# Optimization experiments

Measured on AMD Instinct MI355X. Metric: run time of the kernel, lower is better.

The kernel has to match this reference:

```python
import jax, jax.numpy as jnp
import numpy as np

NUM_REL = 5000
NUM_BIN = 32
NUM_EDGES = 200000
DIM = 512
NUM_HEAD = 8
DIM_HID = DIM // NUM_HEAD


def setup_inputs() -> dict:
    key = jax.random.key(0)
    ks = jax.random.split(key, 10)
    emb_rel = jax.random.normal(ks[0], (NUM_REL, DIM), dtype=jnp.float32)
    emb_bin = jax.random.normal(ks[1], (NUM_BIN, DIM), dtype=jnp.float32)
    head = jax.random.randint(ks[2], (NUM_EDGES, 1), 0, NUM_REL)
    tail = jax.random.randint(ks[3], (NUM_EDGES, 1), 0, NUM_REL)
    bins = jax.random.randint(ks[4], (NUM_EDGES, 1), 0, NUM_BIN)
    relation_triplets = jnp.concatenate([head, tail, bins], axis=1).astype(jnp.int64)
    gain = float(np.sqrt(2.0))  # calculate_gain('relu')
    # xavier normal: std = gain * sqrt(2/(fan_in+fan_out))
    std_attn = gain * np.sqrt(2.0 / (3 * DIM + DIM))
    std_aggr = gain * np.sqrt(2.0 / (DIM + DIM))
    std_vec = gain * np.sqrt(2.0 / (NUM_HEAD + DIM_HID))
    W_attn = std_attn * jax.random.normal(ks[5], (DIM, 3 * DIM), dtype=jnp.float32)
    b_attn = jnp.zeros((DIM,), dtype=jnp.float32)
    attn_vec = std_vec * jax.random.normal(ks[6], (1, NUM_HEAD, DIM_HID), dtype=jnp.float32)
    W_aggr = std_aggr * jax.random.normal(ks[7], (DIM, DIM), dtype=jnp.float32)
    b_aggr = jnp.zeros((DIM,), dtype=jnp.float32)
    return {"emb_rel": emb_rel, "emb_bin": emb_bin, "relation_triplets": relation_triplets,
            "W_attn": W_attn, "b_attn": b_attn, "attn_vec": attn_vec,
            "W_aggr": W_aggr, "b_aggr": b_aggr}


def reference(emb_rel, emb_bin, relation_triplets, W_attn, b_attn, attn_vec, W_aggr, b_aggr):
    num_rel = emb_rel.shape[0]
    head = relation_triplets[:, 0]
    tail = relation_triplets[:, 1]
    bins = relation_triplets[:, 2]
    # gather + concat -> [E, 3*D]
    concat = jnp.concatenate([emb_rel[head], emb_bin[bins], emb_rel[tail]], axis=-1)
    h = jax.nn.leaky_relu(concat @ W_attn.T + b_attn, negative_slope=0.2)
    h = h.reshape(-1, NUM_HEAD, DIM_HID)
    attn_raw = jnp.sum(h * attn_vec, axis=-1)  # [E, H]
    # segmented softmax over edges sharing the same head relation
    seg_max = jax.ops.segment_max(attn_raw, head, num_segments=num_rel)  # [R, H]
    seg_max = jnp.where(jnp.isfinite(seg_max), seg_max, 0.0)  # empty segments
    ev = jnp.exp(attn_raw - seg_max[head])  # [E, H]
    seg_sum = jax.ops.segment_sum(ev, head, num_segments=num_rel)  # [R, H]
    beta = ev / (seg_sum[head] + 1e-16)  # [E, H]
    msg = (emb_rel[tail] @ W_aggr.T + b_aggr).reshape(-1, NUM_HEAD, DIM_HID)  # [E, H, Dh]
    out = jax.ops.segment_sum(beta[..., None] * msg, head, num_segments=num_rel)  # [R, H, Dh]
    return out.reshape(num_rel, -1)
```

## Files before the change

### kernel.cpp

```cpp
#include <hip/hip_runtime.h>
#include <hip/hip_bf16.h>

#define NREL 5000
#define NBIN 32
#define NEDGE 200000
#define DIM 512
#define NHEAD 8
#define CAP 256

typedef __attribute__((ext_vector_type(8))) short short8;
typedef __attribute__((ext_vector_type(4))) short short4v;
typedef __attribute__((ext_vector_type(4))) float f32x4;
typedef unsigned short ushort_t;

#define REL_N (NREL * DIM)
#define BIN_N (NBIN * DIM)
#define WATTN_N (DIM * 3 * DIM)
#define WAGGR_N (DIM * DIM)
#define CTOT (REL_N + BIN_N + WATTN_N + WAGGR_N)
#define CONV_BLOCKS (CTOT / 4 / 256)

__device__ __forceinline__ float b2f(ushort_t u) {
  unsigned int v = ((unsigned int)u) << 16;
  union { unsigned int i; float f; } c; c.i = v; return c.f;
}
__device__ __forceinline__ ushort_t f2b_rne(float f) {
  union { float f; unsigned int u; } c; c.f = f;
  unsigned int u = c.u;
  return (ushort_t)((u + 0x7FFFu + ((u >> 16) & 1u)) >> 16);
}
__device__ __forceinline__ void gload16(const void* g, void* l) {
  __builtin_amdgcn_global_load_lds(
      (const __attribute__((address_space(1))) void*)g,
      (__attribute__((address_space(3))) void*)l, 16, 0, 0);
}

__global__ void conv_k(const float* __restrict__ s_rel, const float* __restrict__ s_bin,
                       const float* __restrict__ s_wattn, const float* __restrict__ s_waggr,
                       ushort_t* __restrict__ dst, int* __restrict__ cur) {
  int b = blockIdx.x;
  if (b < 20) {
    int i = b * 256 + threadIdx.x;
    if (i < NREL) cur[i] = 0;
  }
  const int O1 = REL_N, O2 = O1 + BIN_N, O3 = O2 + WATTN_N;
  int i4 = (b * 256 + threadIdx.x) * 4;
  const float* src; int j;
  if (i4 < O1)      { src = s_rel;   j = i4; }
  else if (i4 < O2) { src = s_bin;   j = i4 - O1; }
  else if (i4 < O3) { src = s_wattn; j = i4 - O2; }
  else              { src = s_waggr; j = i4 - O3; }
  float4 v = *(const float4*)(src + j);
  short4v o;
  o[0] = (short)f2b_rne(v.x); o[1] = (short)f2b_rne(v.y);
  o[2] = (short)f2b_rne(v.z); o[3] = (short)f2b_rne(v.w);
  *(short4v*)(dst + i4) = o;
}

__global__ __launch_bounds__(256) void gemm_scatter_k(
    const ushort_t* __restrict__ c_rel, const ushort_t* __restrict__ c_bin,
    const ushort_t* __restrict__ c_wattn, const float* __restrict__ b_attn,
    const ushort_t* __restrict__ c_waggr, const float* __restrict__ b_aggr,
    ushort_t* __restrict__ P1B, ushort_t* __restrict__ PM, ushort_t* __restrict__ P2,
    const int* __restrict__ trip, int* __restrict__ cur, unsigned int* __restrict__ etb)
{
  __shared__ ushort_t Alds[64 * 64];
  __shared__ ushort_t Blds[128 * 64];
  int bx = blockIdx.x, by = blockIdx.y;
  if (by >= 12) {
    int sid = (by - 12) * 80 + bx;
    for (int i = threadIdx.x; i < 625; i += 256) {
      int e = sid * 625 + i;
      int h  = trip[3 * e];
      int ta = trip[3 * e + 1];
      int bi = trip[3 * e + 2];
      h  = min(max(h, 0), NREL - 1);
      ta = min(max(ta, 0), NREL - 1);
      bi = min(max(bi, 0), NBIN - 1);
      int p = atomicAdd(&cur[h], 1);
      if (p < CAP)
        etb[(h << 8) + p] = ((unsigned int)ta << 11) | ((unsigned int)bi << 24);
    }
    return;
  }
  const ushort_t* A; int Arows;
  const ushort_t* Bbase; int Bld; int joff;
  const float* bias;
  ushort_t* OUT; int OUTld; int ocolOff;
  int rbase;
  if (bx == 79) {
    if (by >= 4) return;
    A = c_bin; Arows = NBIN; rbase = 0;
    Bbase = c_wattn + 512; Bld = 3 * DIM; joff = 0;
    bias = b_attn;
    OUT = P2; OUTld = DIM; ocolOff = 0;
  } else {
    A = c_rel; Arows = NREL; rbase = bx * 64;
    int seg = by >> 2;
    if (seg == 2)      { Bbase = c_waggr;        Bld = DIM;     bias = b_aggr; }
    else if (seg == 1) { Bbase = c_wattn + 1024; Bld = 3 * DIM; bias = nullptr; }
    else               { Bbase = c_wattn;        Bld = 3 * DIM; bias = nullptr; }
    joff = seg * 512;
    OUT = (seg == 0) ? P1B : PM;
    OUTld = (seg == 0) ? DIM : 1024;
    ocolOff = (seg == 0) ? 0 : 512;
  }
  int tid = threadIdx.x;
  int l = tid & 63, wv = tid >> 6;
  int ctb = by * 128;
  int lr = l >> 3;
  int srcslot = (l & 7) ^ lr;
  const ushort_t* aS0; const ushort_t* aS1;
  const ushort_t* bS0; const ushort_t* bS1; const ushort_t* bS2; const ushort_t* bS3;
  {
    int a0 = wv * 16 + 0 * 8 + lr, a1 = wv * 16 + 1 * 8 + lr;
    aS0 = A + (size_t)min(rbase + a0, Arows - 1) * DIM + srcslot * 8;
    aS1 = A + (size_t)min(rbase + a1, Arows - 1) * DIM + srcslot * 8;
    int c0 = wv * 32 + 0 * 8 + lr, c1 = wv * 32 + 1 * 8 + lr,
        c2 = wv * 32 + 2 * 8 + lr, c3 = wv * 32 + 3 * 8 + lr;
    bS0 = Bbase + (size_t)(ctb + c0 - joff) * Bld + srcslot * 8;
    bS1 = Bbase + (size_t)(ctb + c1 - joff) * Bld + srcslot * 8;
    bS2 = Bbase + (size_t)(ctb + c2 - joff) * Bld + srcslot * 8;
    bS3 = Bbase + (size_t)(ctb + c3 - joff) * Bld + srcslot * 8;
  }
  ushort_t* aD0 = Alds + (wv * 16 + 0) * 64;
  ushort_t* aD1 = Alds + (wv * 16 + 8) * 64;
  ushort_t* bD0 = Blds + (wv * 32 + 0) * 64;
  ushort_t* bD1 = Blds + (wv * 32 + 8) * 64;
  ushort_t* bD2 = Blds + (wv * 32 + 16) * 64;
  ushort_t* bD3 = Blds + (wv * 32 + 24) * 64;

  f32x4 acc[4][2] = {};
  for (int kk = 0; kk < DIM; kk += 64) {
    gload16(aS0 + kk, aD0); gload16(aS1 + kk, aD1);
    gload16(bS0 + kk, bD0); gload16(bS1 + kk, bD1);
    gload16(bS2 + kk, bD2); gload16(bS3 + kk, bD3);
    __syncthreads();
#pragma unroll
    for (int ks = 0; ks < 2; ++ks) {
      int sg = ks * 4 + (l >> 4);
      int sw = (sg ^ (l & 7)) * 8;
      short8 aF[4], bF[2];
#pragma unroll
      for (int m2 = 0; m2 < 4; ++m2) {
        int mrow = m2 * 16 + (l & 15);
        aF[m2] = *(const short8*)(Alds + mrow * 64 + sw);
      }
#pragma unroll
      for (int n = 0; n < 2; ++n) {
        int crow = wv * 32 + n * 16 + (l & 15);
        bF[n] = *(const short8*)(Blds + crow * 64 + sw);
      }
#pragma unroll
      for (int m2 = 0; m2 < 4; ++m2)
#pragma unroll
        for (int n = 0; n < 2; ++n)
          acc[m2][n] = __builtin_amdgcn_mfma_f32_16x16x32_bf16(aF[m2], bF[n], acc[m2][n], 0, 0, 0);
    }
    __syncthreads();
  }
  int r0 = rbase + (l >> 4) * 4;
#pragma unroll
  for (int n = 0; n < 2; ++n) {
    int col = ctb + wv * 32 + n * 16 + (l & 15);
    float bv = bias ? bias[col - joff] : 0.0f;
    int ocol = col - ocolOff;
#pragma unroll
    for (int m2 = 0; m2 < 4; ++m2) {
#pragma unroll
      for (int jj = 0; jj < 4; ++jj) {
        int row = r0 + m2 * 16 + jj;
        if (row < Arows) OUT[(size_t)row * OUTld + ocol] = f2b_rne(acc[m2][n][jj] + bv);
      }
    }
  }
}

#define EDGE_LOAD(TB, P2V, P3V, MV)                                     \
  {                                                                     \
    const char* row_ = PMc + ((TB) & 0x00FFFFFFu);                      \
    P2V = *(const short8*)(p2lds + (((TB) >> 24) << 10) + l16);         \
    P3V = *(const short8*)(row_ + l16);                                 \
    MV  = *(const short8*)(row_ + 1024 + l16);                          \
  }

#define EDGE_COMPUTE(P2V, P3V, MV)                                      \
  {                                                                     \
    float part = 0.0f;                                                  \
    _Pragma("unroll")                                                   \
    for (int j = 0; j < 8; ++j) {                                       \
      float z = p1v[j] + b2f((ushort_t)P2V[j]) + b2f((ushort_t)P3V[j]); \
      part += z * (z > 0.f ? avv[j] : avv02[j]);                        \
    }                                                                   \
    part += __shfl_xor(part, 1);                                        \
    part += __shfl_xor(part, 2);                                        \
    part += __shfl_xor(part, 4);                                        \
    if (part > m + 8.0f) {                                              \
      float f = __expf(m - part);                                       \
      s *= f;                                                           \
      _Pragma("unroll")                                                 \
      for (int j = 0; j < 8; ++j) acc[j] *= f;                          \
      m = part;                                                         \
    }                                                                   \
    float ev = __expf(part - m);                                        \
    s += ev;                                                            \
    _Pragma("unroll")                                                   \
    for (int j = 0; j < 8; ++j) acc[j] += ev * b2f((ushort_t)MV[j]);    \
  }

__global__ __launch_bounds__(256, 6) void aggr2_k(
    const int* __restrict__ cur, const unsigned int* __restrict__ etb,
    const ushort_t* __restrict__ P1B, const ushort_t* __restrict__ PM,
    const ushort_t* __restrict__ P2, const float* __restrict__ avec,
    float* __restrict__ outf)
{
  __shared__ __align__(16) char shmem[32 * DIM * 2];

  int t = threadIdx.x;
  int l = t & 63, wv = t >> 6;
  int p = wv >> 1, sub = wv & 1;
  int r = blockIdx.x * 2 + p;
  int nE = min(cur[r], CAP);
  int base = r << 8;
  int half = nE >> 1;
  int start = sub ? half : 0;
  int cnt = sub ? (nE - half) : half;

  int hd1 = l >> 3;
  int ob = l * 8;
  int l16 = l * 16;

  {
    ushort_t* p2dst = (ushort_t*)shmem;
#pragma unroll
    for (int i = 0; i < 8; ++i) {
      int idx = t * 8 + i * 2048;
      *(short8*)(p2dst + idx) = *(const short8*)(P2 + idx);
    }
  }

  float p1v[8], avv[8], avv02[8];
  {
    short8 p1b = *(const short8*)(P1B + (size_t)r * DIM + ob);
#pragma unroll
    for (int j = 0; j < 8; ++j) {
      p1v[j] = b2f((ushort_t)p1b[j]);
      float a = avec[ob + j];
      avv[j] = a;
      avv02[j] = 0.2f * a;
    }
  }
  float acc[8] = {};
  float m = -INFINITY, s = 0.0f;

  const char* PMc = (const char*)PM;
  const char* p2lds = (const char*)shmem;

  __syncthreads();

  for (int ck = 0; ck < cnt; ck += 64) {
    int ne = min(64, cnt - ck);
    unsigned int tbreg = 0;
    if (l < ne) tbreg = etb[base + start + ck + l];
    short8 p2A, p3A, mvA, p2B, p3B, mvB;
    unsigned int tb0 = (unsigned int)__shfl((int)tbreg, 0);
    EDGE_LOAD(tb0, p2A, p3A, mvA);
    int i = 0;
    while (i + 1 < ne) {
      unsigned int tbb = (unsigned int)__shfl((int)tbreg, i + 1);
      EDGE_LOAD(tbb, p2B, p3B, mvB);
      EDGE_COMPUTE(p2A, p3A, mvA);
      if (i + 2 < ne) {
        unsigned int tba = (unsigned int)__shfl((int)tbreg, i + 2);
        EDGE_LOAD(tba, p2A, p3A, mvA);
      }
      EDGE_COMPUTE(p2B, p3B, mvB);
      i += 2;
    }
    if (i < ne) EDGE_COMPUTE(p2A, p3A, mvA);
  }

  __syncthreads();
  float* red = (float*)shmem;
  float* ms  = (float*)(shmem + 8192);
#pragma unroll
  for (int j = 0; j < 8; ++j) red[wv * DIM + ob + j] = acc[j];
  if ((l & 7) == 0) { ms[(wv * NHEAD + hd1) * 2] = m; ms[(wv * NHEAD + hd1) * 2 + 1] = s; }
  __syncthreads();

  int pp = t >> 7;
  int d0 = (t & 127) * 4;
  int h = d0 >> 6;
  int rr = blockIdx.x * 2 + pp;
  float m1 = ms[((2 * pp) * NHEAD + h) * 2],     s1 = ms[((2 * pp) * NHEAD + h) * 2 + 1];
  float m2 = ms[((2 * pp + 1) * NHEAD + h) * 2], s2 = ms[((2 * pp + 1) * NHEAD + h) * 2 + 1];
  float M = fmaxf(m1, m2);
  float c1 = (m1 == M) ? 1.0f : __expf(m1 - M);
  float c2 = (m2 == M) ? 1.0f : __expf(m2 - M);
  float S = s1 * c1 + s2 * c2;
  float inv = 1.0f / (S + 1e-16f);
  float4 val;
  val.x = (red[(2 * pp) * DIM + d0]     * c1 + red[(2 * pp + 1) * DIM + d0]     * c2) * inv;
  val.y = (red[(2 * pp) * DIM + d0 + 1] * c1 + red[(2 * pp + 1) * DIM + d0 + 1] * c2) * inv;
  val.z = (red[(2 * pp) * DIM + d0 + 2] * c1 + red[(2 * pp + 1) * DIM + d0 + 2] * c2) * inv;
  val.w = (red[(2 * pp) * DIM + d0 + 3] * c1 + red[(2 * pp + 1) * DIM + d0 + 3] * c2) * inv;
  *(float4*)(outf + (size_t)rr * DIM + d0) = val;
}

extern "C" void kernel_launch(void* const* d_in, const int* in_sizes, int n_in,
                              void* d_out, int out_size, void* d_ws, size_t ws_size,
                              hipStream_t stream) {
  const float* s_rel   = (const float*)d_in[0];
  const float* s_bin   = (const float*)d_in[1];
  const int*   trip    = (const int*)d_in[2];
  const float* s_wattn = (const float*)d_in[3];
  const float* b_attn  = (const float*)d_in[4];
  const float* avec    = (const float*)d_in[5];
  const float* s_waggr = (const float*)d_in[6];
  const float* b_aggr  = (const float*)d_in[7];

  ushort_t* canon = (ushort_t*)d_ws;
  ushort_t* c_rel   = canon;
  ushort_t* c_bin   = c_rel + REL_N;
  ushort_t* c_wattn = c_bin + BIN_N;
  ushort_t* c_waggr = c_wattn + WATTN_N;
  int* cur = (int*)(c_waggr + WAGGR_N);
  unsigned int* etb = (unsigned int*)(cur + NREL);
  ushort_t* P1B = (ushort_t*)(((uintptr_t)(etb + NREL * CAP) + 15) & ~(uintptr_t)15);
  ushort_t* PM  = P1B + (size_t)NREL * DIM;
  ushort_t* P2  = PM + (size_t)NREL * 1024;

  conv_k<<<CONV_BLOCKS, 256, 0, stream>>>(s_rel, s_bin, s_wattn, s_waggr, canon, cur);

  dim3 gg(80, 16);
  gemm_scatter_k<<<gg, 256, 0, stream>>>(c_rel, c_bin, c_wattn, b_attn, c_waggr, b_aggr,
                                         P1B, PM, P2, trip, cur, etb);

  aggr2_k<<<NREL / 2, 256, 0, stream>>>(cur, etb, P1B, PM, P2, avec, (float*)d_out);
}
```

Measured before the change: 82.38 us.

## Split fused online-softmax aggregation into logit pass and weighted-sum pass

The single online-softmax aggregation kernel is split in two. The first kernel computes attention logits per edge, writes them to a workspace buffer and produces a per-relation max and sum. The second kernel rereads the edge list and the message rows and accumulates already-normalized weights, so the running rescale of the accumulators is no longer needed. In exchange it adds a kernel launch, rereads etb, PM rows and the logits from memory, and halves CAP to 128, which silently drops edges for any relation with more than 128 incoming edges.

Measured after the change: 97.96 us. 18.9% more time.

```diff
diff --git a/kernel.cpp b/kernel.cpp
--- a/kernel.cpp
+++ b/kernel.cpp
@@ -6,7 +6,7 @@
 #define NEDGE 200000
 #define DIM 512
 #define NHEAD 8
-#define CAP 256
+#define CAP 128
 
 typedef __attribute__((ext_vector_type(8))) short short8;
 typedef __attribute__((ext_vector_type(4))) short short4v;
@@ -79,7 +79,7 @@
       bi = min(max(bi, 0), NBIN - 1);
       int p = atomicAdd(&cur[h], 1);
       if (p < CAP)
-        etb[(h << 8) + p] = ((unsigned int)ta << 11) | ((unsigned int)bi << 24);
+        etb[h * CAP + p] = ((unsigned int)ta << 11) | ((unsigned int)bi << 24);
     }
     return;
   }
@@ -176,15 +176,14 @@
   }
 }
 
-#define EDGE_LOAD(TB, P2V, P3V, MV)                                     \
+#define EDGE_LOAD_A(TB, P2V, P3V)                                       \
   {                                                                     \
     const char* row_ = PMc + ((TB) & 0x00FFFFFFu);                      \
     P2V = *(const short8*)(p2lds + (((TB) >> 24) << 10) + l16);         \
     P3V = *(const short8*)(row_ + l16);                                 \
-    MV  = *(const short8*)(row_ + 1024 + l16);                          \
-  }
-
-#define EDGE_COMPUTE(P2V, P3V, MV)                                      \
+  }
+
+#define EDGE_COMPUTE_A(P2V, P3V, SLOT)                                  \
   {                                                                     \
     float part = 0.0f;                                                  \
     _Pragma("unroll")                                                   \
@@ -196,23 +195,18 @@
     part += __shfl_xor(part, 2);                                        \
     part += __shfl_xor(part, 4);                                        \
     if (part > m + 8.0f) {                                              \
-      float f = __expf(m - part);                                       \
-      s *= f;                                                           \
-      _Pragma("unroll")                                                 \
-      for (int j = 0; j < 8; ++j) acc[j] *= f;                          \
+      s *= __expf(m - part);                                            \
       m = part;                                                         \
     }                                                                   \
-    float ev = __expf(part - m);                                        \
-    s += ev;                                                            \
-    _Pragma("unroll")                                                   \
-    for (int j = 0; j < 8; ++j) acc[j] += ev * b2f((ushort_t)MV[j]);    \
-  }
-
-__global__ __launch_bounds__(256, 6) void aggr2_k(
+    s += __expf(part - m);                                              \
+    if ((l & 7) == 0) LG[(SLOT) * 8 + hd1] = part;                      \
+  }
+
+__global__ __launch_bounds__(256, 6) void aggrA_k(
     const int* __restrict__ cur, const unsigned int* __restrict__ etb,
     const ushort_t* __restrict__ P1B, const ushort_t* __restrict__ PM,
     const ushort_t* __restrict__ P2, const float* __restrict__ avec,
-    float* __restrict__ outf)
+    float* __restrict__ LG, float2* __restrict__ mshS)
 {
   __shared__ __align__(16) char shmem[32 * DIM * 2];
 
@@ -221,7 +215,7 @@
   int p = wv >> 1, sub = wv & 1;
   int r = blockIdx.x * 2 + p;
   int nE = min(cur[r], CAP);
-  int base = r << 8;
+  int base = r * CAP;
   int half = nE >> 1;
   int start = sub ? half : 0;
   int cnt = sub ? (nE - half) : half;
@@ -250,7 +244,6 @@
       avv02[j] = 0.2f * a;
     }
   }
-  float acc[8] = {};
   float m = -INFINITY, s = 0.0f;
 
   const char* PMc = (const char*)PM;
@@ -262,48 +255,117 @@
     int ne = min(64, cnt - ck);
     unsigned int tbreg = 0;
     if (l < ne) tbreg = etb[base + start + ck + l];
-    short8 p2A, p3A, mvA, p2B, p3B, mvB;
+    short8 p2A, p3A, p2B, p3B;
     unsigned int tb0 = (unsigned int)__shfl((int)tbreg, 0);
-    EDGE_LOAD(tb0, p2A, p3A, mvA);
+    EDGE_LOAD_A(tb0, p2A, p3A);
     int i = 0;
     while (i + 1 < ne) {
       unsigned int tbb = (unsigned int)__shfl((int)tbreg, i + 1);
-      EDGE_LOAD(tbb, p2B, p3B, mvB);
-      EDGE_COMPUTE(p2A, p3A, mvA);
+      EDGE_LOAD_A(tbb, p2B, p3B);
+      EDGE_COMPUTE_A(p2A, p3A, base + start + ck + i);
       if (i + 2 < ne) {
         unsigned int tba = (unsigned int)__shfl((int)tbreg, i + 2);
-        EDGE_LOAD(tba, p2A, p3A, mvA);
+        EDGE_LOAD_A(tba, p2A, p3A);
       }
-      EDGE_COMPUTE(p2B, p3B, mvB);
+      EDGE_COMPUTE_A(p2B, p3B, base + start + ck + i + 1);
       i += 2;
     }
-    if (i < ne) EDGE_COMPUTE(p2A, p3A, mvA);
+    if (i < ne) EDGE_COMPUTE_A(p2A, p3A, base + start + ck + i);
   }
 
   __syncthreads();
-  float* red = (float*)shmem;
-  float* ms  = (float*)(shmem + 8192);
-#pragma unroll
-  for (int j = 0; j < 8; ++j) red[wv * DIM + ob + j] = acc[j];
+  float* ms = (float*)shmem;
   if ((l & 7) == 0) { ms[(wv * NHEAD + hd1) * 2] = m; ms[(wv * NHEAD + hd1) * 2 + 1] = s; }
   __syncthreads();
+  if (t < 16) {
+    int pp = t >> 3, h = t & 7;
+    float m1 = ms[((2 * pp) * NHEAD + h) * 2],     s1 = ms[((2 * pp) * NHEAD + h) * 2 + 1];
+    float m2 = ms[((2 * pp + 1) * NHEAD + h) * 2], s2 = ms[((2 * pp + 1) * NHEAD + h) * 2 + 1];
+    float M = fmaxf(m1, m2);
+    float c1 = (m1 == M) ? 1.0f : __expf(m1 - M);
+    float c2 = (m2 == M) ? 1.0f : __expf(m2 - M);
+    float2 v; v.x = M; v.y = s1 * c1 + s2 * c2;
+    mshS[(blockIdx.x * 2 + pp) * NHEAD + h] = v;
+  }
+}
+
+#define EDGE_LOAD_B(TB, SLOT, MV, LGV)                                  \
+  {                                                                     \
+    const char* row_ = PMc + ((TB) & 0x00FFFFFFu);                      \
+    MV  = *(const short8*)(row_ + 1024 + l16);                          \
+    LGV = LG[(SLOT) * 8 + hd1];                                        \
+  }
+
+#define EDGE_COMPUTE_B(MV, LGV)                                         \
+  {                                                                     \
+    float w = __expf(LGV - M) * invS;                                   \
+    _Pragma("unroll")                                                   \
+    for (int j = 0; j < 8; ++j) acc[j] += w * b2f((ushort_t)MV[j]);     \
+  }
+
+__global__ __launch_bounds__(256, 8) void aggrB_k(
+    const int* __restrict__ cur, const unsigned int* __restrict__ etb,
+    const ushort_t* __restrict__ PM, const float* __restrict__ LG,
+    const float2* __restrict__ mshS, float* __restrict__ outf)
+{
+  __shared__ __align__(16) float red[4][DIM];
+
+  int t = threadIdx.x;
+  int l = t & 63, wv = t >> 6;
+  int p = wv >> 1, sub = wv & 1;
+  int r = blockIdx.x * 2 + p;
+  int nE = min(cur[r], CAP);
+  int base = r * CAP;
+  int half = nE >> 1;
+  int start = sub ? half : 0;
+  int cnt = sub ? (nE - half) : half;
+
+  int hd1 = l >> 3;
+  int ob = l * 8;
+  int l16 = l * 16;
+
+  float2 msv = mshS[r * NHEAD + hd1];
+  float M = msv.x;
+  float invS = 1.0f / (msv.y + 1e-16f);
+
+  float acc[8] = {};
+  const char* PMc = (const char*)PM;
+
+  for (int ck = 0; ck < cnt; ck += 64) {
+    int ne = min(64, cnt - ck);
+    unsigned int tbreg = 0;
+    if (l < ne) tbreg = etb[base + start + ck + l];
+    short8 mvA, mvB;
+    float lgA, lgB;
+    unsigned int tb0 = (unsigned int)__shfl((int)tbreg, 0);
+    EDGE_LOAD_B(tb0, base + start + ck, mvA, lgA);
+    int i = 0;
+    while (i + 1 < ne) {
+      unsigned int tbb = (unsigned int)__shfl((int)tbreg, i + 1);
+      EDGE_LOAD_B(tbb, base + start + ck + i + 1, mvB, lgB);
+      EDGE_COMPUTE_B(mvA, lgA);
+      if (i + 2 < ne) {
+        unsigned int tba = (unsigned int)__shfl((int)tbreg, i + 2);
+        EDGE_LOAD_B(tba, base + start + ck + i + 2, mvA, lgA);
+      }
+      EDGE_COMPUTE_B(mvB, lgB);
+      i += 2;
+    }
+    if (i < ne) EDGE_COMPUTE_B(mvA, lgA);
+  }
+
+#pragma unroll
+  for (int j = 0; j < 8; ++j) red[wv][ob + j] = acc[j];
+  __syncthreads();
 
   int pp = t >> 7;
   int d0 = (t & 127) * 4;
-  int h = d0 >> 6;
   int rr = blockIdx.x * 2 + pp;
-  float m1 = ms[((2 * pp) * NHEAD + h) * 2],     s1 = ms[((2 * pp) * NHEAD + h) * 2 + 1];
-  float m2 = ms[((2 * pp + 1) * NHEAD + h) * 2], s2 = ms[((2 * pp + 1) * NHEAD + h) * 2 + 1];
-  float M = fmaxf(m1, m2);
-  float c1 = (m1 == M) ? 1.0f : __expf(m1 - M);
-  float c2 = (m2 == M) ? 1.0f : __expf(m2 - M);
-  float S = s1 * c1 + s2 * c2;
-  float inv = 1.0f / (S + 1e-16f);
   float4 val;
-  val.x = (red[(2 * pp) * DIM + d0]     * c1 + red[(2 * pp + 1) * DIM + d0]     * c2) * inv;
-  val.y = (red[(2 * pp) * DIM + d0 + 1] * c1 + red[(2 * pp + 1) * DIM + d0 + 1] * c2) * inv;
-  val.z = (red[(2 * pp) * DIM + d0 + 2] * c1 + red[(2 * pp + 1) * DIM + d0 + 2] * c2) * inv;
-  val.w = (red[(2 * pp) * DIM + d0 + 3] * c1 + red[(2 * pp + 1) * DIM + d0 + 3] * c2) * inv;
+  val.x = red[2 * pp][d0]     + red[2 * pp + 1][d0];
+  val.y = red[2 * pp][d0 + 1] + red[2 * pp + 1][d0 + 1];
+  val.z = red[2 * pp][d0 + 2] + red[2 * pp + 1][d0 + 2];
+  val.w = red[2 * pp][d0 + 3] + red[2 * pp + 1][d0 + 3];
   *(float4*)(outf + (size_t)rr * DIM + d0) = val;
 }
 
@@ -329,6 +391,8 @@
   ushort_t* P1B = (ushort_t*)(((uintptr_t)(etb + NREL * CAP) + 15) & ~(uintptr_t)15);
   ushort_t* PM  = P1B + (size_t)NREL * DIM;
   ushort_t* P2  = PM + (size_t)NREL * 1024;
+  float* LG     = (float*)(P2 + NBIN * DIM);
+  float2* mshS  = (float2*)(LG + (size_t)NREL * CAP * 8);
 
   conv_k<<<CONV_BLOCKS, 256, 0, stream>>>(s_rel, s_bin, s_wattn, s_waggr, canon, cur);
 
@@ -336,5 +400,6 @@
   gemm_scatter_k<<<gg, 256, 0, stream>>>(c_rel, c_bin, c_wattn, b_attn, c_waggr, b_aggr,
                                          P1B, PM, P2, trip, cur, etb);
 
-  aggr2_k<<<NREL / 2, 256, 0, stream>>>(cur, etb, P1B, PM, P2, avec, (float*)d_out);
-}
+  aggrA_k<<<NREL / 2, 256, 0, stream>>>(cur, etb, P1B, PM, P2, avec, LG, mshS);
+  aggrB_k<<<NREL / 2, 256, 0, stream>>>(cur, etb, PM, LG, mshS, (float*)d_out);
+}
```
